# Optimization experiments

Hardware: AMD Instinct MI355X
Metric: run time of the kernel (lower is better)

Reference implementation:

```python
import jax, jax.numpy as jnp
import numpy as np

B, N = 16, 16          # batch, boxes per image
H, W = 640, 640        # image size
PH, PW = 300, 300      # learned patch size
MIN_AREA = 60.0
MAX_ANG = 20.0 * np.pi / 180.0


def setup_inputs() -> dict:
    key = jax.random.key(0)
    k1, k2, k3 = jax.random.split(key, 3)
    images = jax.random.uniform(k1, (B, H, W, 3), jnp.float32, -1.0, 1.0)
    patch = jax.random.uniform(k2, (PH, PW, 3), jnp.float32, -1.0, 1.0)
    kb1, kb2, kb3 = jax.random.split(k3, 3)
    ymin = jax.random.uniform(kb1, (B, N), jnp.float32, 0.0, H - 220.0)
    xmin = jax.random.uniform(kb2, (B, N), jnp.float32, 0.0, W - 220.0)
    hw = jax.random.uniform(kb3, (B, N, 2), jnp.float32, 100.0, 200.0)
    boxes = jnp.stack([ymin, xmin, ymin + hw[..., 0], xmin + hw[..., 1]], axis=-1)
    scale = jnp.float32(0.4)
    return {"boxes": boxes, "images": images, "patch": patch, "scale": scale}


def _bilinear(img, ys, xs):
    # img [Ph,Pw,3]; ys,xs [H,W] continuous source coords -> [H,W,3]
    Ph, Pw = img.shape[0], img.shape[1]
    y0 = jnp.floor(ys)
    x0 = jnp.floor(xs)
    wy = (ys - y0)[..., None]
    wx = (xs - x0)[..., None]
    y0i = jnp.clip(y0.astype(jnp.int32), 0, Ph - 1)
    y1i = jnp.clip(y0i + 1, 0, Ph - 1)
    x0i = jnp.clip(x0.astype(jnp.int32), 0, Pw - 1)
    x1i = jnp.clip(x0i + 1, 0, Pw - 1)
    v00 = img[y0i, x0i]
    v01 = img[y0i, x1i]
    v10 = img[y1i, x0i]
    v11 = img[y1i, x1i]
    return v00 * (1 - wy) * (1 - wx) + v01 * (1 - wy) * wx + v10 * wy * (1 - wx) + v11 * wy * wx


def _per_image(img, boxes_i, patch, scale, key):
    # random_print_adjust: per-channel affine jitter of the patch
    kw, kb, kloop = jax.random.split(key, 3)
    w = jax.random.normal(kw, (1, 1, 3), jnp.float32) * 0.1 + 0.5
    b = jax.random.normal(kb, (1, 1, 3), jnp.float32) * 0.01
    p = jnp.clip(w * patch + b, -1.0, 1.0)
    # BrightnessMatcher: shift patch mean brightness to match the image
    p = jnp.clip(p + (jnp.mean(img) - jnp.mean(p)), -1.0, 1.0)

    oimg = img
    mask0 = jnp.zeros_like(img)
    yy, xx = jnp.meshgrid(jnp.arange(H, dtype=jnp.float32),
                          jnp.arange(W, dtype=jnp.float32), indexing="ij")

    def step(carry, inp):
        image, mask = carry
        box, kk = inp
        ymin, xmin, ymax, xmax = box[0], box[1], box[2], box[3]
        h = ymax - ymin
        ww = xmax - xmin
        longer = jnp.maximum(h, ww)
        ps = jnp.floor(longer * scale)                       # patch_h == patch_w
        diag = jnp.minimum(jnp.sqrt(2.0).astype(jnp.float32) * ps, jnp.float32(W))
        oy = ymin + h / 2.0
        ox = xmin + ww / 2.0
        y0 = jnp.maximum(oy - diag / 2.0, 0.0)
        x0 = jnp.maximum(ox - diag / 2.0, 0.0)
        y0 = jnp.where(y0 + diag > H, H - diag, y0)
        x0 = jnp.where(x0 + diag > W, W - diag, x0)
        # int casts as in the TF code (values are >= 0, trunc == floor)
        y0i = jnp.floor(y0)
        x0i = jnp.floor(x0)
        phi = jnp.maximum(jnp.floor(ps), 1.0)
        diagi = jnp.floor(diag)
        valid_box = (phi * phi) > MIN_AREA

        k1, k2, k3 = jax.random.split(kk, 3)
        angle = jax.random.uniform(k1, (), jnp.float32, -MAX_ANG, MAX_ANG)

        # inverse warp: output pixel -> padded-patch coords -> resized-patch coords
        u = yy - y0i
        v = xx - x0i
        in_sq = (u >= 0) & (v >= 0) & (u < diagi) & (v < diagi)
        c = (diagi - 1.0) / 2.0
        ca, sa = jnp.cos(angle), jnp.sin(angle)
        su = c + ca * (u - c) - sa * (v - c)
        sv = c + sa * (u - c) + ca * (v - c)
        top = jnp.floor((diagi - phi) / 2.0)   # pad offset (floor top/left)
        py = su - top
        px = sv - top
        valid_src = (py >= 0) & (py <= phi - 1) & (px >= 0) & (px <= phi - 1)
        # resized-patch coords -> original patch coords (bilinear resize, half-pixel)
        sy = (py + 0.5) * (PH / phi) - 0.5
        sx = (px + 0.5) * (PW / phi) - 0.5
        samp = _bilinear(p, sy, sx)                                   # [H,W,3]
        noise = jax.random.uniform(k2, samp.shape, jnp.float32, -0.1, 0.1)
        bright = jax.random.uniform(k3, (), jnp.float32, -0.3, 0.3)
        im = jnp.clip(samp + noise + bright, -1.0, 1.0)
        val = jnp.where(valid_src[..., None], im, -2.0)
        val = jnp.where(val < -1.0, image, val)   # fill with current background
        val = jnp.clip(val, -1.0, 1.0)
        sel = (in_sq & valid_box)[..., None]
        new_image = jnp.where(sel, val, image)
        new_mask = jnp.where(sel, oimg - val, mask)
        return (new_image, new_mask), None

    keys = jax.random.split(kloop, N)
    (img_out, mask_out), _ = jax.lax.scan(step, (img, mask0), (boxes_i, keys))
    return img_out, mask_out


def reference(boxes, images, patch, scale):
    keys = jax.random.split(jax.random.key(42), B)
    img_out, mask_out = jax.vmap(_per_image, in_axes=(0, 0, None, None, 0))(
        images, boxes, patch, scale, keys)
    return img_out, mask_out
```

## Files before the change

### kernel.cpp

```cpp
#include <hip/hip_runtime.h>
#include <stdint.h>
#include <math.h>

#define B_ 16
#define N_ 16
#define H_ 640
#define W_ 640
#define PH_ 300
#define PW_ 300

#define IMG_ELEMS (H_*W_*3)
#define PATCH_ELEMS (PH_*PW_*3)

typedef float f32x4 __attribute__((ext_vector_type(4)));

__device__ __forceinline__ uint2 tf2x32(uint32_t k0, uint32_t k1, uint32_t x0, uint32_t x1) {
  uint32_t k2 = k0 ^ k1 ^ 0x1BD11BDAu;
#define TFR(r) x0 += x1; x1 = (x1 << (r)) | (x1 >> (32 - (r))); x1 ^= x0;
  x0 += k0; x1 += k1;
  TFR(13) TFR(15) TFR(26) TFR(6)
  x0 += k1; x1 += k2 + 1u;
  TFR(17) TFR(29) TFR(16) TFR(24)
  x0 += k2; x1 += k0 + 2u;
  TFR(13) TFR(15) TFR(26) TFR(6)
  x0 += k0; x1 += k1 + 3u;
  TFR(17) TFR(29) TFR(16) TFR(24)
  x0 += k1; x1 += k2 + 4u;
  TFR(13) TFR(15) TFR(26) TFR(6)
  x0 += k2; x1 += k0 + 5u;
#undef TFR
  return make_uint2(x0, x1);
}

__device__ __forceinline__ uint32_t rb32(uint32_t k0, uint32_t k1, uint32_t i) {
  uint2 o = tf2x32(k0, k1, 0u, i);
  return o.x ^ o.y;
}

__device__ __forceinline__ float u01f(uint32_t bits) {
  return __uint_as_float((bits >> 9) | 0x3F800000u) - 1.0f;
}

__device__ __forceinline__ float erfinv32(float x) {
  float w = -log1pf(-x * x);
  float p;
  if (w < 5.0f) {
    w = w - 2.5f;
    p = 2.81022636e-08f;
    p = fmaf(p, w, 3.43273939e-07f);
    p = fmaf(p, w, -3.5233877e-06f);
    p = fmaf(p, w, -4.39150654e-06f);
    p = fmaf(p, w, 0.00021858087f);
    p = fmaf(p, w, -0.00125372503f);
    p = fmaf(p, w, -0.00417768164f);
    p = fmaf(p, w, 0.246640727f);
    p = fmaf(p, w, 1.50140941f);
  } else {
    w = sqrtf(w) - 3.0f;
    p = -0.000200214257f;
    p = fmaf(p, w, 0.000100950558f);
    p = fmaf(p, w, 0.00134934322f);
    p = fmaf(p, w, -0.00367342844f);
    p = fmaf(p, w, 0.00573950773f);
    p = fmaf(p, w, -0.0076224613f);
    p = fmaf(p, w, 0.00943887047f);
    p = fmaf(p, w, 1.00167406f);
    p = fmaf(p, w, 2.83297682f);
  }
  return p * x;
}

__device__ __forceinline__ float jnormal(uint32_t bits) {
  float lo = __uint_as_float(0xBF7FFFFFu);
  float span = 1.0f - lo;
  float u = fmaxf(lo, u01f(bits) * span + lo);
  return 1.4142135623730951f * erfinv32(u);
}

__global__ void setup_kernel(const float* __restrict__ boxes, const float* __restrict__ scale_p,
                             float* __restrict__ params, float* __restrict__ wb) {
  int t = threadIdx.x;
  if (t >= B_*N_) return;
  int b = t >> 4, n = t & 15;
  uint2 kb = tf2x32(0u, 42u, 0u, (uint32_t)b);
  uint2 kw  = tf2x32(kb.x, kb.y, 0u, 0u);
  uint2 kbk = tf2x32(kb.x, kb.y, 0u, 1u);
  uint2 kl  = tf2x32(kb.x, kb.y, 0u, 2u);
  if (n == 0) {
    wb[b*8+0] = jnormal(rb32(kw.x,  kw.y,  0u)) * 0.1f + 0.5f;
    wb[b*8+1] = jnormal(rb32(kw.x,  kw.y,  1u)) * 0.1f + 0.5f;
    wb[b*8+2] = jnormal(rb32(kw.x,  kw.y,  2u)) * 0.1f + 0.5f;
    wb[b*8+3] = jnormal(rb32(kbk.x, kbk.y, 0u)) * 0.01f;
    wb[b*8+4] = jnormal(rb32(kbk.x, kbk.y, 1u)) * 0.01f;
    wb[b*8+5] = jnormal(rb32(kbk.x, kbk.y, 2u)) * 0.01f;
  }
  uint2 kk = tf2x32(kl.x, kl.y, 0u, (uint32_t)n);
  uint2 k1 = tf2x32(kk.x, kk.y, 0u, 0u);
  uint2 k2 = tf2x32(kk.x, kk.y, 0u, 1u);
  uint2 k3 = tf2x32(kk.x, kk.y, 0u, 2u);
  const float MA = (float)(20.0 * 3.14159265358979323846 / 180.0);
  float angle  = fmaxf(-MA,   u01f(rb32(k1.x, k1.y, 0u)) * (MA - (-MA)) + (-MA));
  float bright = fmaxf(-0.3f, u01f(rb32(k3.x, k3.y, 0u)) * (0.3f - (-0.3f)) + (-0.3f));

  const float* bx = boxes + (size_t)t * 4;
  float ymin = bx[0], xmin = bx[1], ymax = bx[2], xmax = bx[3];
  float sc = scale_p[0];
  float h = ymax - ymin, ww = xmax - xmin;
  float longer = fmaxf(h, ww);
  float ps = floorf(longer * sc);
  float diag = fminf(sqrtf(2.0f) * ps, (float)W_);
  float oy = ymin + h * 0.5f;
  float ox = xmin + ww * 0.5f;
  float y0 = fmaxf(oy - diag * 0.5f, 0.0f);
  float x0 = fmaxf(ox - diag * 0.5f, 0.0f);
  if (y0 + diag > (float)H_) y0 = (float)H_ - diag;
  if (x0 + diag > (float)W_) x0 = (float)W_ - diag;
  float y0i = floorf(y0), x0i = floorf(x0);
  float phi = fmaxf(floorf(ps), 1.0f);
  float diagi = floorf(diag);
  float validf = ((phi * phi) > 60.0f) ? 1.0f : 0.0f;
  float c = (diagi - 1.0f) * 0.5f;
  float top = floorf((diagi - phi) * 0.5f);

  float* P = params + t * 16;
  P[0] = y0i; P[1] = x0i; P[2] = diagi; P[3] = phi;
  P[4] = c;
  P[5] = (float)cos((double)angle);
  P[6] = (float)sin((double)angle);
  P[7] = top;
  P[8] = bright; P[9] = (float)PH_ / phi; P[10] = 0.0f; P[11] = validf;
  P[12] = __uint_as_float(k2.x); P[13] = __uint_as_float(k2.y); P[14] = 0.0f; P[15] = 0.0f;
}

__global__ __launch_bounds__(256) void reduce_kernel(
    const float* __restrict__ images, const float* __restrict__ patch,
    const float* __restrict__ wb, double* __restrict__ partials) {
  int b = blockIdx.y, j = blockIdx.x, t = threadIdx.x;
  const float* img = images + (size_t)b * IMG_ELEMS;
  double s = 0.0;
  for (int i = j * 256 + t; i < IMG_ELEMS; i += 64 * 256) s += (double)img[i];
  float w0 = wb[b*8+0], w1 = wb[b*8+1], w2 = wb[b*8+2];
  float b0 = wb[b*8+3], b1 = wb[b*8+4], b2 = wb[b*8+5];
  double sp = 0.0;
  for (int i = j * 256 + t; i < PATCH_ELEMS; i += 64 * 256) {
    int q = i / 3; int ch = i - q * 3;
    float wv = (ch == 0) ? w0 : ((ch == 1) ? w1 : w2);
    float bv = (ch == 0) ? b0 : ((ch == 1) ? b1 : b2);
    float pv = fminf(fmaxf(wv * patch[i] + bv, -1.0f), 1.0f);
    sp += (double)pv;
  }
  __shared__ double sh[256];
  sh[t] = s; __syncthreads();
  for (int o = 128; o > 0; o >>= 1) { if (t < o) sh[t] += sh[t + o]; __syncthreads(); }
  if (t == 0) partials[((size_t)b * 64 + j) * 2 + 0] = sh[0];
  __syncthreads();
  sh[t] = sp; __syncthreads();
  for (int o = 128; o > 0; o >>= 1) { if (t < o) sh[t] += sh[t + o]; __syncthreads(); }
  if (t == 0) partials[((size_t)b * 64 + j) * 2 + 1] = sh[0];
}

__global__ void finalize_kernel(const double* __restrict__ partials, float* __restrict__ dvals) {
  int t = threadIdx.x;
  if (t < B_) {
    double si = 0.0, sp = 0.0;
    for (int j = 0; j < 64; j++) {
      si += partials[((size_t)t * 64 + j) * 2 + 0];
      sp += partials[((size_t)t * 64 + j) * 2 + 1];
    }
    float mi = (float)(si / (double)IMG_ELEMS);
    float mp = (float)(sp / (double)PATCH_ELEMS);
    dvals[t] = mi - mp;
  }
}

__global__ __launch_bounds__(256) void patch_adjust_kernel(
    const float* __restrict__ patch, const float* __restrict__ wb,
    const float* __restrict__ dvals, float* __restrict__ padj) {
  int b = blockIdx.y;
  float w0 = wb[b*8+0], w1 = wb[b*8+1], w2 = wb[b*8+2];
  float b0 = wb[b*8+3], b1 = wb[b*8+4], b2 = wb[b*8+5];
  float dsh = dvals[b];
  float* dst = padj + (size_t)b * PATCH_ELEMS;
  int i0 = (blockIdx.x * 256 + threadIdx.x) * 4;
  if (i0 + 3 >= PATCH_ELEMS && i0 >= PATCH_ELEMS) return;
  if (i0 + 4 <= PATCH_ELEMS) {
    f32x4 pv = *(const f32x4*)(patch + i0);
    float o[4];
#pragma unroll
    for (int e = 0; e < 4; e++) {
      int ch = (i0 + e) % 3;
      float wv = (ch == 0) ? w0 : ((ch == 1) ? w1 : w2);
      float bv = (ch == 0) ? b0 : ((ch == 1) ? b1 : b2);
      float a = fminf(fmaxf(wv * pv[e] + bv, -1.0f), 1.0f);
      o[e] = fminf(fmaxf(a + dsh, -1.0f), 1.0f);
    }
    f32x4 ov = {o[0], o[1], o[2], o[3]};
    *(f32x4*)(dst + i0) = ov;
  }
}

template<int PADJ>
__global__ __launch_bounds__(256) void main_kernel(
    const float* __restrict__ images, const float* __restrict__ patchsrc,
    const float* __restrict__ params, const float* __restrict__ wb,
    const float* __restrict__ dvals, float* __restrict__ out) {
  __shared__ float sP[N_ * 16];
  __shared__ float sWB[6];
  __shared__ int sList[N_];
  __shared__ int sCount;

  int bid = blockIdx.x;
  int b  = (bid & 7) * 2 + ((bid >> 3) & 1);
  int pb = bid >> 4;
  int tid = threadIdx.x;

  if (tid < N_ * 16) sP[tid] = params[b * N_ * 16 + tid];
  if (PADJ == 0 && tid < 6) sWB[tid] = wb[b * 8 + tid];
  if (tid == 0) {
    const float* Pb = params + b * N_ * 16;
    int pblk = pb * 1024;
    int ys = pblk / W_;
    int ye = (pblk + 1023) / W_;
    int cnt = 0;
    for (int n = 0; n < N_; n++) {
      const float* P = Pb + n * 16;
      if (P[11] == 0.0f) continue;
      float fy0 = P[0];
      float fy1 = P[0] + P[2] - 1.0f;
      if (fy1 < (float)ys || fy0 > (float)ye) continue;
      sList[cnt++] = n;
    }
    sCount = cnt;
  }
  __syncthreads();

  int lane = tid & 63;
  int wv   = tid >> 6;
  int span = pb * 1024 + wv * 256;
  size_t ibase = (size_t)b * (H_ * W_) * 3;
  const float* patchb = PADJ ? (patchsrc + (size_t)b * PATCH_ELEMS) : patchsrc;
  float dsh = PADJ ? 0.0f : dvals[b];

  int   pj[4];  float yfj[4], xfj[4];
#pragma unroll
  for (int j = 0; j < 4; j++) {
    int p = span + j * 64 + lane;
    int chunk = span + j * 64;
    int y = chunk / W_;
    pj[j]  = p;
    yfj[j] = (float)y;
    xfj[j] = (float)(chunk - y * W_ + lane);
  }

  float orig[12], img[12], mk[12];
#pragma unroll
  for (int j = 0; j < 4; j++) {
    const float* src = images + ibase + (size_t)pj[j] * 3;
    orig[j*3+0] = __builtin_nontemporal_load(src + 0);
    orig[j*3+1] = __builtin_nontemporal_load(src + 1);
    orig[j*3+2] = __builtin_nontemporal_load(src + 2);
  }
#pragma unroll
  for (int e = 0; e < 12; e++) { img[e] = orig[e]; mk[e] = 0.0f; }

  int cnt = sCount;
  for (int li = 0; li < cnt; li++) {
    const float* P = sP + sList[li] * 16;
    float P0 = P[0], P1 = P[1], diagi = P[2];
    float phi = P[3], c = P[4], ca = P[5], sa = P[6], top = P[7], bright = P[8], sph = P[9];
    uint32_t k2a = __float_as_uint(P[12]);
    uint32_t k2b = __float_as_uint(P[13]);
#pragma unroll
    for (int j = 0; j < 4; j++) {
      float u = yfj[j] - P0;
      if (!(u >= 0.0f && u < diagi)) continue;
      float v = xfj[j] - P1;
      if (!(v >= 0.0f && v < diagi)) continue;
      float t1 = u - c, t2 = v - c;
      float su = (c + ca * t1) - sa * t2;
      float sv = (c + sa * t1) + ca * t2;
      float py = su - top;
      float px = sv - top;
      bool vsrc = (py >= 0.0f) && (py <= phi - 1.0f) && (px >= 0.0f) && (px <= phi - 1.0f);
      if (vsrc) {
        float sy = (py + 0.5f) * sph - 0.5f;
        float sx = (px + 0.5f) * sph - 0.5f;
        float fy = floorf(sy), fx = floorf(sx);
        float wy = sy - fy, wxv = sx - fx;
        int iy0 = min(max((int)fy, 0), PH_ - 1);
        int iy1 = min(iy0 + 1, PH_ - 1);
        int ix0 = min(max((int)fx, 0), PW_ - 1);
        int ix1 = min(ix0 + 1, PW_ - 1);
        int o00 = (iy0 * PW_ + ix0) * 3;
        int o01 = (iy0 * PW_ + ix1) * 3;
        int o10 = (iy1 * PW_ + ix0) * 3;
        int o11 = (iy1 * PW_ + ix1) * 3;
        float omwy = 1.0f - wy, omwx = 1.0f - wxv;
        int nbase = pj[j] * 3;
#pragma unroll
        for (int ch = 0; ch < 3; ch++) {
          float a00, a01, a10, a11;
          if (PADJ) {
            a00 = patchb[o00 + ch];
            a01 = patchb[o01 + ch];
            a10 = patchb[o10 + ch];
            a11 = patchb[o11 + ch];
          } else {
            float wv2 = sWB[ch], bv = sWB[3 + ch];
            a00 = fminf(fmaxf(wv2 * patchb[o00 + ch] + bv, -1.0f), 1.0f);
            a01 = fminf(fmaxf(wv2 * patchb[o01 + ch] + bv, -1.0f), 1.0f);
            a10 = fminf(fmaxf(wv2 * patchb[o10 + ch] + bv, -1.0f), 1.0f);
            a11 = fminf(fmaxf(wv2 * patchb[o11 + ch] + bv, -1.0f), 1.0f);
            a00 = fminf(fmaxf(a00 + dsh, -1.0f), 1.0f);
            a01 = fminf(fmaxf(a01 + dsh, -1.0f), 1.0f);
            a10 = fminf(fmaxf(a10 + dsh, -1.0f), 1.0f);
            a11 = fminf(fmaxf(a11 + dsh, -1.0f), 1.0f);
          }
          float samp = ((a00 * omwy) * omwx) + ((a01 * omwy) * wxv)
                     + ((a10 * wy) * omwx) + ((a11 * wy) * wxv);
          int i = nbase + ch;
          uint32_t bits = rb32(k2a, k2b, (uint32_t)i);
          float nz = fmaxf(-0.1f, u01f(bits) * (0.1f - (-0.1f)) + (-0.1f));
          float imv = fminf(fmaxf((samp + nz) + bright, -1.0f), 1.0f);
          img[j * 3 + ch] = imv;
          mk[j * 3 + ch] = orig[j * 3 + ch] - imv;
        }
      } else {
#pragma unroll
        for (int ch = 0; ch < 3; ch++) mk[j * 3 + ch] = orig[j * 3 + ch] - img[j * 3 + ch];
      }
    }
  }

  size_t moff = (size_t)B_ * (H_ * W_) * 3;
#pragma unroll
  for (int j = 0; j < 4; j++) {
    float* od = out + ibase + (size_t)pj[j] * 3;
    float* md = od + moff;
#pragma unroll
    for (int ch = 0; ch < 3; ch++) {
      __builtin_nontemporal_store(img[j*3+ch], od + ch);
      __builtin_nontemporal_store(mk[j*3+ch],  md + ch);
    }
  }
}

extern "C" void kernel_launch(void* const* d_in, const int* in_sizes, int n_in,
                              void* d_out, int out_size, void* d_ws, size_t ws_size,
                              hipStream_t stream) {
  const float* boxes  = (const float*)d_in[0];
  const float* images = (const float*)d_in[1];
  const float* patch  = (const float*)d_in[2];
  const float* scale  = (const float*)d_in[3];
  float* out = (float*)d_out;

  float* params = (float*)d_ws;
  float* wb     = params + B_ * N_ * 16;
  float* dvals  = wb + B_ * 8;
  double* partials = (double*)((char*)d_ws + 20480);
  float* padj   = (float*)((char*)d_ws + 36864);
  const size_t PADJ_NEED = 36864 + (size_t)B_ * PATCH_ELEMS * 4;

  setup_kernel<<<1, 256, 0, stream>>>(boxes, scale, params, wb);
  reduce_kernel<<<dim3(64, B_), 256, 0, stream>>>(images, patch, wb, partials);
  finalize_kernel<<<1, 64, 0, stream>>>(partials, dvals);
  if (ws_size >= PADJ_NEED) {
    patch_adjust_kernel<<<dim3((PATCH_ELEMS + 1023) / 1024, B_), 256, 0, stream>>>(
        patch, wb, dvals, padj);
    main_kernel<1><<<(H_ * W_ * B_) / 1024, 256, 0, stream>>>(
        images, padj, params, wb, dvals, out);
  } else {
    main_kernel<0><<<(H_ * W_ * B_) / 1024, 256, 0, stream>>>(
        images, patch, params, wb, dvals, out);
  }
}
```

Measured before the change: 298.1 us.

## Use 2D pixel tiles with box culling and vectorized copy fast path

Main kernel blocks now cover 16x64 2D tiles instead of 1024-pixel linear spans. Each block culls boxes by both x and y extent, so fewer boxes reach the per-pixel loop. Tiles hit by no box take a fast path that copies the image with vector loads and writes zeros to the mask using 16-byte nontemporal stores. The column-dependent box test is hoisted out of the row loop. In exchange, stores from each wave now cover shorter contiguous row segments, and original-image loads no longer use nontemporal hints.

After: 293.0 us. No clear change (-1.7%).

```diff
diff --git a/kernel.cpp b/kernel.cpp
--- a/kernel.cpp
+++ b/kernel.cpp
@@ -11,6 +11,12 @@
 
 #define IMG_ELEMS (H_*W_*3)
 #define PATCH_ELEMS (PH_*PW_*3)
+
+#define TROWS 16
+#define TCOLS 64
+#define TILES_Y (H_/TROWS)
+#define TILES_X (W_/TCOLS)
+#define TILES_PER_IMG (TILES_Y*TILES_X)
 
 typedef float f32x4 __attribute__((ext_vector_type(4)));
 
@@ -182,7 +188,6 @@
   float dsh = dvals[b];
   float* dst = padj + (size_t)b * PATCH_ELEMS;
   int i0 = (blockIdx.x * 256 + threadIdx.x) * 4;
-  if (i0 + 3 >= PATCH_ELEMS && i0 >= PATCH_ELEMS) return;
   if (i0 + 4 <= PATCH_ELEMS) {
     f32x4 pv = *(const f32x4*)(patch + i0);
     float o[4];
@@ -211,23 +216,24 @@
 
   int bid = blockIdx.x;
   int b  = (bid & 7) * 2 + ((bid >> 3) & 1);
-  int pb = bid >> 4;
+  int tl = bid >> 4;
+  int ty = tl / TILES_X;
+  int tx = tl - ty * TILES_X;
   int tid = threadIdx.x;
 
   if (tid < N_ * 16) sP[tid] = params[b * N_ * 16 + tid];
   if (PADJ == 0 && tid < 6) sWB[tid] = wb[b * 8 + tid];
   if (tid == 0) {
     const float* Pb = params + b * N_ * 16;
-    int pblk = pb * 1024;
-    int ys = pblk / W_;
-    int ye = (pblk + 1023) / W_;
+    float ys = (float)(ty * TROWS), ye = (float)(ty * TROWS + TROWS - 1);
+    float xs = (float)(tx * TCOLS), xe = (float)(tx * TCOLS + TCOLS - 1);
     int cnt = 0;
     for (int n = 0; n < N_; n++) {
       const float* P = Pb + n * 16;
       if (P[11] == 0.0f) continue;
-      float fy0 = P[0];
-      float fy1 = P[0] + P[2] - 1.0f;
-      if (fy1 < (float)ys || fy0 > (float)ye) continue;
+      float last = P[2] - 1.0f;
+      if (P[0] + last < ys || P[0] > ye) continue;
+      if (P[1] + last < xs || P[1] > xe) continue;
       sList[cnt++] = n;
     }
     sCount = cnt;
@@ -236,29 +242,42 @@
 
   int lane = tid & 63;
   int wv   = tid >> 6;
-  int span = pb * 1024 + wv * 256;
-  size_t ibase = (size_t)b * (H_ * W_) * 3;
+  size_t ibase = (size_t)b * IMG_ELEMS;
+  size_t moff  = (size_t)B_ * IMG_ELEMS;
+
+  if (sCount == 0) {
+    const f32x4 z = {0.0f, 0.0f, 0.0f, 0.0f};
+#pragma unroll
+    for (int k = 0; k < 3; k++) {
+      int t4 = k * 64 + lane;
+      int r  = t4 / 48;
+      int c  = t4 - r * 48;
+      int row = ty * TROWS + wv * 4 + r;
+      size_t fbase = ibase + ((size_t)row * W_ + tx * TCOLS) * 3 + (size_t)c * 4;
+      f32x4 d = *(const f32x4*)(images + fbase);
+      __builtin_nontemporal_store(d, (f32x4*)(out + fbase));
+      __builtin_nontemporal_store(z, (f32x4*)(out + moff + fbase));
+    }
+    return;
+  }
+
   const float* patchb = PADJ ? (patchsrc + (size_t)b * PATCH_ELEMS) : patchsrc;
   float dsh = PADJ ? 0.0f : dvals[b];
 
-  int   pj[4];  float yfj[4], xfj[4];
+  int   pj[4];  float yfj[4];
+  float xf = (float)(tx * TCOLS + lane);
 #pragma unroll
   for (int j = 0; j < 4; j++) {
-    int p = span + j * 64 + lane;
-    int chunk = span + j * 64;
-    int y = chunk / W_;
-    pj[j]  = p;
-    yfj[j] = (float)y;
-    xfj[j] = (float)(chunk - y * W_ + lane);
+    int row = ty * TROWS + wv * 4 + j;
+    pj[j]  = row * W_ + tx * TCOLS + lane;
+    yfj[j] = (float)row;
   }
 
   float orig[12], img[12], mk[12];
 #pragma unroll
   for (int j = 0; j < 4; j++) {
     const float* src = images + ibase + (size_t)pj[j] * 3;
-    orig[j*3+0] = __builtin_nontemporal_load(src + 0);
-    orig[j*3+1] = __builtin_nontemporal_load(src + 1);
-    orig[j*3+2] = __builtin_nontemporal_load(src + 2);
+    orig[j*3+0] = src[0]; orig[j*3+1] = src[1]; orig[j*3+2] = src[2];
   }
 #pragma unroll
   for (int e = 0; e < 12; e++) { img[e] = orig[e]; mk[e] = 0.0f; }
@@ -270,13 +289,15 @@
     float phi = P[3], c = P[4], ca = P[5], sa = P[6], top = P[7], bright = P[8], sph = P[9];
     uint32_t k2a = __float_as_uint(P[12]);
     uint32_t k2b = __float_as_uint(P[13]);
+    float v = xf - P1;
+    bool vok = (v >= 0.0f && v < diagi);
+    float t2 = v - c;
 #pragma unroll
     for (int j = 0; j < 4; j++) {
       float u = yfj[j] - P0;
       if (!(u >= 0.0f && u < diagi)) continue;
-      float v = xfj[j] - P1;
-      if (!(v >= 0.0f && v < diagi)) continue;
-      float t1 = u - c, t2 = v - c;
+      if (!vok) continue;
+      float t1 = u - c;
       float su = (c + ca * t1) - sa * t2;
       float sv = (c + sa * t1) + ca * t2;
       float py = su - top;
@@ -332,7 +353,6 @@
     }
   }
 
-  size_t moff = (size_t)B_ * (H_ * W_) * 3;
 #pragma unroll
   for (int j = 0; j < 4; j++) {
     float* od = out + ibase + (size_t)pj[j] * 3;
@@ -367,10 +387,10 @@
   if (ws_size >= PADJ_NEED) {
     patch_adjust_kernel<<<dim3((PATCH_ELEMS + 1023) / 1024, B_), 256, 0, stream>>>(
         patch, wb, dvals, padj);
-    main_kernel<1><<<(H_ * W_ * B_) / 1024, 256, 0, stream>>>(
+    main_kernel<1><<<B_ * TILES_PER_IMG, 256, 0, stream>>>(
         images, padj, params, wb, dvals, out);
   } else {
-    main_kernel<0><<<(H_ * W_ * B_) / 1024, 256, 0, stream>>>(
+    main_kernel<0><<<B_ * TILES_PER_IMG, 256, 0, stream>>>(
         images, patch, params, wb, dvals, out);
   }
 }
```
